# Kernel optimization log

Hardware: AMD Instinct MI355X
Metric: run time of the kernel (lower is better)

Reference implementation:

```python
import jax, jax.numpy as jnp
import numpy as np

B, T, C = 4, 1024, 1024
NH, L, DHR, FF = 16, 512, 64, 4096
DK = C // NH  # 64
EPS = 1e-6
NEG = -9e15


def rms_norm(x, w):
    var = jnp.mean(jnp.square(x), axis=-1, keepdims=True)
    return x * jax.lax.rsqrt(var + EPS) * w


def rope_apply(x):
    # Faithful to RoPE module: freq = t+1, pos pairs repeated, theta = exp(-2*pos/C*ln(1e4))
    b, t, c = x.shape
    xf = x.astype(jnp.float32)
    freq = jnp.arange(t, dtype=jnp.float32)[:, None] + 1.0           # [t,1]
    pos = jnp.arange(c // 2, dtype=jnp.float32)[:, None]
    pos = jnp.repeat(pos, 2, axis=-1).reshape(1, -1)                 # [1,c] -> p0,p0,p1,p1,...
    theta = jnp.exp(-2.0 * pos / c * jnp.log(10000.0))
    cos = jnp.cos(freq * theta)                                      # [t,c]
    sin = jnp.sin(freq * theta)
    x2 = xf.reshape(b, t, c // 2, 2)
    rot = jnp.stack([-x2[..., 1], x2[..., 0]], axis=-1).reshape(b, t, c)
    return (xf * cos + rot * sin).astype(x.dtype)


def setup_inputs() -> dict:
    key = jax.random.key(0)
    ks = jax.random.split(key, 12)
    s = 0.02
    return {
        "x": jax.random.normal(ks[0], (B, T, C), jnp.float32),
        "rms1": jnp.ones((C,), jnp.float32),
        "rms2": jnp.ones((C,), jnp.float32),
        "W_dkv": s * jax.random.normal(ks[1], (C, 2 * L), jnp.float32),
        "b_dkv": jnp.zeros((2 * L,), jnp.float32),
        "W_kr": s * jax.random.normal(ks[2], (2 * L, DHR), jnp.float32),
        "b_kr": jnp.zeros((DHR,), jnp.float32),
        "W_qr": s * jax.random.normal(ks[3], (2 * L, DHR * NH), jnp.float32),
        "b_qr": jnp.zeros((DHR * NH,), jnp.float32),
        "W_kv": s * jax.random.normal(ks[4], (L, 2 * C), jnp.float32),
        "b_kv": jnp.zeros((2 * C,), jnp.float32),
        "W_q": s * jax.random.normal(ks[5], (L, C), jnp.float32),
        "b_q": jnp.zeros((C,), jnp.float32),
        "W_o": s * jax.random.normal(ks[6], (C, C), jnp.float32),
        "b_o": jnp.zeros((C,), jnp.float32),
        "W_f1": s * jax.random.normal(ks[7], (C, FF), jnp.float32),
        "b_f1": jnp.zeros((FF,), jnp.float32),
        "W_f2": s * jax.random.normal(ks[8], (FF, C), jnp.float32),
        "b_f2": jnp.zeros((C,), jnp.float32),
    }


def mla(x, W_dkv, b_dkv, W_kr, b_kr, W_qr, b_qr, W_kv, b_kv, W_q, b_q, W_o, b_o):
    b, t, c = x.shape
    comp = jnp.einsum('btc,cd->btd', x, W_dkv) + b_dkv               # [B,T,2L]
    cKV, cq = jnp.split(comp, 2, axis=-1)                            # [B,T,L] each
    # RoPE branches (computed from the compressed representation, as in source)
    kR = rope_apply(jnp.einsum('btl,ld->btd', comp, W_kr) + b_kr)    # [B,T,DHR]
    qR = rope_apply(jnp.einsum('btl,ld->btd', comp, W_qr) + b_qr)    # roped over full NH*DHR dim
    qR = qR.reshape(b, t, NH, DHR).transpose(0, 2, 1, 3)             # [B,NH,T,DHR]
    kv = jnp.einsum('btl,ld->btd', cKV, W_kv) + b_kv
    k, v = jnp.split(kv, 2, axis=-1)                                 # [B,T,C] each
    q = jnp.einsum('btl,ld->btd', cq, W_q) + b_q                     # [B,T,C]
    to_heads = lambda z: z.reshape(b, t, NH, DK).transpose(0, 2, 1, 3)
    q, k, v = to_heads(q), to_heads(k), to_heads(v)                  # [B,NH,T,DK]
    q = jnp.concatenate([q, qR], axis=-1)                            # [B,NH,T,DK+DHR]
    k = jnp.concatenate([k, jnp.broadcast_to(kR[:, None], (b, NH, t, DHR))], axis=-1)
    # manual masked softmax in fp32, scale uses DK (not DK+DHR), faithful to source
    scale = 1.0 / np.sqrt(DK)
    w = jnp.einsum('bnqd,bnkd->bnqk', q.astype(jnp.float32), k.astype(jnp.float32)) * scale
    mask = jnp.tril(jnp.ones((t, t), jnp.float32))
    w = jnp.where(mask == 0, NEG, w)
    p = jax.nn.softmax(w, axis=-1)
    o = jnp.einsum('bnqk,bnkd->bnqd', p, v.astype(jnp.float32)).astype(x.dtype)
    o = o.transpose(0, 2, 1, 3).reshape(b, t, c)
    return jnp.einsum('btc,cd->btd', o, W_o) + b_o


def ffn(x, W_f1, b_f1, W_f2, b_f2):
    h = jax.nn.gelu(jnp.einsum('btc,cf->btf', x, W_f1) + b_f1)
    return jnp.einsum('btf,fc->btc', h, W_f2) + b_f2


def reference(x, rms1, rms2, W_dkv, b_dkv, W_kr, b_kr, W_qr, b_qr,
              W_kv, b_kv, W_q, b_q, W_o, b_o, W_f1, b_f1, W_f2, b_f2):
    h = x + mla(rms_norm(x, rms1), W_dkv, b_dkv, W_kr, b_kr, W_qr, b_qr,
                W_kv, b_kv, W_q, b_q, W_o, b_o)
    out = h + ffn(rms_norm(h, rms2), W_f1, b_f1, W_f2, b_f2)
    return out
```

## Files before the change

kernel.cpp:

```cpp
#include <hip/hip_runtime.h>

typedef unsigned int u32;
typedef unsigned short u16;
typedef __bf16 bf16x8 __attribute__((ext_vector_type(8)));
typedef float f32x4 __attribute__((ext_vector_type(4)));

#define B_ 4
#define T_ 1024
#define C_ 1024
#define NH_ 16
#define L_ 512
#define DHR_ 64
#define FF_ 4096

typedef __attribute__((address_space(3))) u32 as3_u32;
typedef __attribute__((address_space(1))) u32 as1_u32;

__device__ __forceinline__ void gld16(const u16* g, u16* l) {
  __builtin_amdgcn_global_load_lds((const as1_u32*)g, (as3_u32*)l, 16, 0, 0);
}

__device__ __forceinline__ float bf2f(u16 u) {
  union { u32 i; float f; } v; v.i = ((u32)u) << 16; return v.f;
}
__device__ __forceinline__ u16 f2bf(float f) {
  union { float f; u32 i; } v; v.f = f;
  u32 r = (v.i + 0x7FFFu + ((v.i >> 16) & 1u)) >> 16;
  return (u16)r;
}

struct TransArgs {
  const float* src[8];
  u16* dst[8];
  int R[8], C[8];
  int base[9];
};

__global__ void transpose_all(TransArgs ta) {
  __shared__ float tile[32][33];
  const int bid = blockIdx.x;
  int w = 0;
#pragma unroll
  for (int i = 1; i < 8; i++) w += (bid >= ta.base[i]);
  const int local = bid - ta.base[w];
  const int R = ta.R[w], C = ta.C[w];
  const int ctiles = C >> 5;
  const int bx = (local % ctiles) * 32;
  const int by = (local / ctiles) * 32;
  const float* in = ta.src[w];
  u16* outp = ta.dst[w];
  const int tx = threadIdx.x, ty = threadIdx.y;
  for (int i = ty; i < 32; i += 8)
    tile[i][tx] = in[(size_t)(by + i) * C + bx + tx];
  __syncthreads();
  for (int i = ty; i < 32; i += 8)
    outp[(size_t)(bx + i) * R + by + tx] = f2bf(tile[tx][i]);
}

__global__ __launch_bounds__(256) void rmsnorm_kernel(const float* __restrict__ xin,
                                                      const float* __restrict__ w,
                                                      u16* __restrict__ outp) {
  const int row = blockIdx.x;
  const int tid = threadIdx.x;
  const float* xp = xin + (size_t)row * C_;
  float v[4];
#pragma unroll
  for (int i = 0; i < 4; i++) v[i] = xp[tid + 256 * i];
  float ss = v[0] * v[0] + v[1] * v[1] + v[2] * v[2] + v[3] * v[3];
#pragma unroll
  for (int o = 32; o > 0; o >>= 1) ss += __shfl_down(ss, o, 64);
  __shared__ float red[4];
  if ((tid & 63) == 0) red[tid >> 6] = ss;
  __syncthreads();
  ss = red[0] + red[1] + red[2] + red[3];
  float scale = rsqrtf(ss * (1.0f / 1024.0f) + 1e-6f);
  u16* op = outp + (size_t)row * C_;
#pragma unroll
  for (int i = 0; i < 4; i++)
    op[tid + 256 * i] = f2bf(v[i] * scale * w[tid + 256 * i]);
}

template<int EPI, bool NCLIP>
__device__ __forceinline__ void g128_body(
    u16* As, u16* Bs,
    const u16* __restrict__ A, int lda, int aoff,
    const u16* __restrict__ BT, const float* __restrict__ bias,
    const float* __restrict__ resid, void* __restrict__ out,
    int N, int Kfull, int Klen, int m0, int n0, int koff) {
  const int tid = threadIdx.x;
  const int wave = tid >> 6, lane = tid & 63;
  const int wm = wave >> 1, wn = wave & 1;
  const int quad = lane >> 4, l15 = lane & 15;
  const int row = tid >> 2, seg = tid & 3;

  const u16* aP = A + (size_t)(m0 + row) * lda + aoff + koff + seg * 8;
  const u16* bP = BT + (size_t)(n0 + row) * Kfull + koff + seg * 8;
  u16* aL = As + row * 32 + seg * 8;
  u16* bL = Bs + row * 32 + seg * 8;
  const size_t aStep = (size_t)64 * lda;
  const size_t bStep = (size_t)64 * Kfull;

  f32x4 acc[4][4] = {};

  for (int k0 = 0; k0 < Klen; k0 += 32) {
    gld16(aP + k0, aL);
    gld16(aP + k0 + aStep, aL + 64 * 32);
    gld16(bP + k0, bL);
    gld16(bP + k0 + bStep, bL + 64 * 32);
    __syncthreads();
    bf16x8 af[4], bf[4];
#pragma unroll
    for (int mt = 0; mt < 4; mt++)
      af[mt] = *(const bf16x8*)&As[(wm * 64 + mt * 16 + l15) * 32 + quad * 8];
#pragma unroll
    for (int nt = 0; nt < 4; nt++)
      bf[nt] = *(const bf16x8*)&Bs[(wn * 64 + nt * 16 + l15) * 32 + quad * 8];
#pragma unroll
    for (int mt = 0; mt < 4; mt++)
#pragma unroll
      for (int nt = 0; nt < 4; nt++)
        acc[mt][nt] = __builtin_amdgcn_mfma_f32_16x16x32_bf16(af[mt], bf[nt], acc[mt][nt], 0, 0, 0);
    __syncthreads();
  }

#pragma unroll
  for (int nt = 0; nt < 4; nt++) {
    const int gn = n0 + wn * 64 + nt * 16 + l15;
    if (NCLIP && gn >= N) continue;
    const float bvv = (EPI == 4) ? 0.0f : bias[gn];
#pragma unroll
    for (int mt = 0; mt < 4; mt++) {
#pragma unroll
      for (int i = 0; i < 4; i++) {
        const int gm = m0 + wm * 64 + mt * 16 + quad * 4 + i;
        const size_t oidx = (size_t)gm * N + gn;
        float v = acc[mt][nt][i] + bvv;
        if (EPI == 2) {
          float xg = v;
          v = 0.5f * xg * (1.0f + tanhf(0.7978845608028654f * (xg + 0.044715f * xg * xg * xg)));
        }
        if (EPI == 3) v += resid[oidx];
        if (EPI == 1 || EPI == 3 || EPI == 4) ((float*)out)[oidx] = v;
        else ((u16*)out)[oidx] = f2bf(v);
      }
    }
  }
}

template<int EPI>
__global__ __launch_bounds__(256) void gemm128(
    const u16* __restrict__ A, int lda, int aoff,
    const u16* __restrict__ BT, const float* __restrict__ bias,
    const float* __restrict__ resid, void* __restrict__ out,
    int M, int N, int K) {
  __shared__ __align__(16) u16 As[128 * 32];
  __shared__ __align__(16) u16 Bs[128 * 32];
  g128_body<EPI, false>(As, Bs, A, lda, aoff, BT, bias, resid, out,
                        N, K, K, blockIdx.x * 128, blockIdx.y * 128, 0);
}

__global__ __launch_bounds__(256) void gemm128_splitk(
    const u16* __restrict__ A, int lda, const u16* __restrict__ BT,
    float* __restrict__ part, int N, int Kfull, int Klen) {
  __shared__ __align__(16) u16 As[128 * 32];
  __shared__ __align__(16) u16 Bs[128 * 32];
  const int z = blockIdx.z;
  g128_body<4, false>(As, Bs, A, lda, 0, BT, nullptr, nullptr,
                      part + (size_t)z * 4096 * N,
                      N, Kfull, Klen, blockIdx.x * 128, blockIdx.y * 128, z * Klen);
}

__global__ __launch_bounds__(256) void f2_reduce(
    const float* __restrict__ part, const float* __restrict__ h,
    const float* __restrict__ bias, float* __restrict__ out) {
  const size_t base = (size_t)blockIdx.x * 1024;
  const size_t PS = (size_t)4096 * 1024;
#pragma unroll
  for (int i = 0; i < 4; i++) {
    const int col = threadIdx.x + 256 * i;
    out[base + col] = h[base + col] + bias[col] + part[base + col] +
                      part[PS + base + col] + part[2 * PS + base + col] +
                      part[3 * PS + base + col];
  }
}

__global__ __launch_bounds__(256) void proj_fused(
    const u16* __restrict__ comp,
    const u16* __restrict__ WT_qr, const float* __restrict__ b_qr, float* __restrict__ qr_pre,
    const u16* __restrict__ WT_kr, const float* __restrict__ b_kr, float* __restrict__ kr_pre,
    const u16* __restrict__ WT_kv, const float* __restrict__ b_kv, u16* __restrict__ kvbuf,
    const u16* __restrict__ WT_q, const float* __restrict__ b_q, u16* __restrict__ qbuf) {
  __shared__ __align__(16) u16 As[128 * 32];
  __shared__ __align__(16) u16 Bs[128 * 32];
  const int m0 = blockIdx.x * 128;
  const int ny = blockIdx.y;
  if (ny < 8)
    g128_body<1, false>(As, Bs, comp, 1024, 0, WT_qr, b_qr, nullptr, qr_pre, 1024, 1024, 1024, m0, ny * 128, 0);
  else if (ny == 8)
    g128_body<1, true>(As, Bs, comp, 1024, 0, WT_kr, b_kr, nullptr, kr_pre, 64, 1024, 1024, m0, 0, 0);
  else if (ny < 25)
    g128_body<0, false>(As, Bs, comp, 1024, 0, WT_kv, b_kv, nullptr, kvbuf, 2048, 512, 512, m0, (ny - 9) * 128, 0);
  else
    g128_body<0, false>(As, Bs, comp, 1024, 512, WT_q, b_q, nullptr, qbuf, 1024, 512, 512, m0, (ny - 25) * 128, 0);
}

__global__ __launch_bounds__(256) void rope_build(
    const u16* __restrict__ qb, const float* __restrict__ qr_pre,
    const u16* __restrict__ kvb, const float* __restrict__ kr_pre,
    u16* __restrict__ Qf, u16* __restrict__ Kf) {
  const int bt = blockIdx.x;
  const int b = bt >> 10, t = bt & 1023;
  const float freq = (float)(t + 1);
  for (int idx = threadIdx.x; idx < 2048; idx += 256) {
    const int h = idx >> 7, d = idx & 127;
    const size_t dst = (((size_t)(b * 16 + h)) * T_ + t) * 128 + d;
    u16 qv, kvv;
    if (d < 64) {
      qv = qb[(size_t)bt * C_ + h * 64 + d];
      kvv = kvb[(size_t)bt * 2048 + h * 64 + d];
    } else {
      const int dd = d - 64;
      {
        const int g = h * 64 + dd;
        const int p = g >> 1;
        const float theta = __expf(-(float)(2 * p) * (9.210340372f / 1024.0f));
        float s, c;
        sincosf(freq * theta, &s, &c);
        const float x0 = qr_pre[(size_t)bt * 1024 + (p << 1)];
        const float x1 = qr_pre[(size_t)bt * 1024 + (p << 1) + 1];
        qv = f2bf((g & 1) ? (x1 * c + x0 * s) : (x0 * c - x1 * s));
      }
      {
        const int p = dd >> 1;
        const float theta = __expf(-(float)(2 * p) * (9.210340372f / 64.0f));
        float s, c;
        sincosf(freq * theta, &s, &c);
        const float x0 = kr_pre[(size_t)bt * 64 + (p << 1)];
        const float x1 = kr_pre[(size_t)bt * 64 + (p << 1) + 1];
        kvv = f2bf((dd & 1) ? (x1 * c + x0 * s) : (x0 * c - x1 * s));
      }
    }
    Qf[dst] = qv;
    Kf[dst] = kvv;
  }
}

__global__ __launch_bounds__(256) void vtrans_kernel(
    const u16* __restrict__ kvb, u16* __restrict__ Vf) {
  __shared__ u16 tile[64][72];
  const int bh = blockIdx.x, t0 = blockIdx.y * 64;
  const int b = bh >> 4, h = bh & 15;
  const int r = threadIdx.x >> 2, seg = (threadIdx.x & 3) * 16;
  const u16* src = &kvb[((size_t)(b * 1024) + t0 + r) * 2048 + 1024 + h * 64 + seg];
  *(uint4*)&tile[r][seg] = *(const uint4*)src;
  *(uint4*)&tile[r][seg + 8] = *(const uint4*)(src + 8);
  __syncthreads();
  const int d = threadIdx.x >> 2, ts = (threadIdx.x & 3) * 16;
  u16 tmp[16];
#pragma unroll
  for (int j = 0; j < 16; j++) tmp[j] = tile[ts + j][d];
  u16* dst = &Vf[((size_t)bh * 64 + d) * 1024 + t0 + ts];
  *(uint4*)dst = *(uint4*)tmp;
  *(uint4*)(dst + 8) = *(uint4*)(tmp + 8);
}

#define KSTR 136
#define VSTR 72

__device__ __forceinline__ void attn_tile(
    u16* Ks, u16* Vt, u16* Ps,
    const u16* __restrict__ Qf, const u16* __restrict__ Kf,
    const u16* __restrict__ Vf, u16* __restrict__ attn_o,
    int b, int h, int qt) {
  const int tid = threadIdx.x;
  const int wave = tid >> 6, lane = tid & 63;
  const int quad = lane >> 4, l15 = lane & 15;
  const int q0 = qt * 64;
  const size_t bh = (size_t)(b * 16 + h);

  bf16x8 qfrag[4];
  {
    const u16* qb = &Qf[(bh * T_ + q0 + wave * 16 + l15) * 128 + quad * 8];
#pragma unroll
    for (int kc = 0; kc < 4; kc++) qfrag[kc] = *(const bf16x8*)(qb + kc * 32);
  }

  f32x4 acc_o[4] = {};
  float m_i[4], l_i[4];
#pragma unroll
  for (int i = 0; i < 4; i++) { m_i[i] = -3.0e38f; l_i[i] = 0.0f; }

  const int kr_ = tid >> 3, kcs = (tid & 7) * 16;
  const int vd = tid >> 2, vts = (tid & 3) * 16;
  u16* Pw = Ps + wave * 16 * VSTR;

  for (int kt = 0; kt <= qt; kt++) {
    __syncthreads();
    {
      const u16* s0 = &Kf[(bh * T_ + kt * 64 + kr_) * 128 + kcs];
      const u16* s1 = s0 + 32 * 128;
      *(uint4*)&Ks[kr_ * KSTR + kcs] = *(const uint4*)s0;
      *(uint4*)&Ks[kr_ * KSTR + kcs + 8] = *(const uint4*)(s0 + 8);
      *(uint4*)&Ks[(kr_ + 32) * KSTR + kcs] = *(const uint4*)s1;
      *(uint4*)&Ks[(kr_ + 32) * KSTR + kcs + 8] = *(const uint4*)(s1 + 8);
      const u16* vs = &Vf[(bh * 64 + vd) * 1024 + kt * 64 + vts];
      *(uint4*)&Vt[vd * VSTR + vts] = *(const uint4*)vs;
      *(uint4*)&Vt[vd * VSTR + vts + 8] = *(const uint4*)(vs + 8);
    }
    __syncthreads();

    f32x4 acc_s[4] = {};
#pragma unroll
    for (int kc = 0; kc < 4; kc++) {
#pragma unroll
      for (int ng = 0; ng < 4; ng++) {
        bf16x8 bb = *(const bf16x8*)&Ks[(ng * 16 + l15) * KSTR + kc * 32 + quad * 8];
        acc_s[ng] = __builtin_amdgcn_mfma_f32_16x16x32_bf16(qfrag[kc], bb, acc_s[ng], 0, 0, 0);
      }
    }

    float sv[4][4];
#pragma unroll
    for (int ng = 0; ng < 4; ng++)
#pragma unroll
      for (int i = 0; i < 4; i++) {
        float s = acc_s[ng][i] * 0.125f;
        if (kt == qt && (ng * 16 + l15) > (wave * 16 + quad * 4 + i)) s = -3.0e38f;
        sv[ng][i] = s;
      }

    float alpha[4], mx[4];
#pragma unroll
    for (int i = 0; i < 4; i++) {
      float m = fmaxf(fmaxf(sv[0][i], sv[1][i]), fmaxf(sv[2][i], sv[3][i]));
#pragma unroll
      for (int off = 1; off < 16; off <<= 1) m = fmaxf(m, __shfl_xor(m, off, 64));
      float mn = fmaxf(m_i[i], m);
      alpha[i] = __expf(m_i[i] - mn);
      m_i[i] = mn;
      mx[i] = mn;
    }
    float rs[4] = {0.f, 0.f, 0.f, 0.f};
#pragma unroll
    for (int ng = 0; ng < 4; ng++)
#pragma unroll
      for (int i = 0; i < 4; i++) {
        float p = __expf(sv[ng][i] - mx[i]);
        rs[i] += p;
        Pw[(quad * 4 + i) * VSTR + ng * 16 + l15] = f2bf(p);
      }
#pragma unroll
    for (int i = 0; i < 4; i++) {
      float r = rs[i];
#pragma unroll
      for (int off = 1; off < 16; off <<= 1) r += __shfl_xor(r, off, 64);
      l_i[i] = l_i[i] * alpha[i] + r;
    }

#pragma unroll
    for (int ng = 0; ng < 4; ng++)
#pragma unroll
      for (int i = 0; i < 4; i++) acc_o[ng][i] *= alpha[i];
#pragma unroll
    for (int kc = 0; kc < 2; kc++) {
      bf16x8 a = *(const bf16x8*)&Pw[l15 * VSTR + kc * 32 + quad * 8];
#pragma unroll
      for (int ng = 0; ng < 4; ng++) {
        bf16x8 bb = *(const bf16x8*)&Vt[(ng * 16 + l15) * VSTR + kc * 32 + quad * 8];
        acc_o[ng] = __builtin_amdgcn_mfma_f32_16x16x32_bf16(a, bb, acc_o[ng], 0, 0, 0);
      }
    }
  }

  float linv[4];
#pragma unroll
  for (int i = 0; i < 4; i++) linv[i] = 1.0f / l_i[i];
#pragma unroll
  for (int ng = 0; ng < 4; ng++)
#pragma unroll
    for (int i = 0; i < 4; i++) {
      const int qrow = q0 + wave * 16 + quad * 4 + i;
      attn_o[((size_t)(b * T_) + qrow) * C_ + h * 64 + ng * 16 + l15] =
          f2bf(acc_o[ng][i] * linv[i]);
    }
}

__global__ __launch_bounds__(256) void attn_mfma(
    const u16* __restrict__ Qf, const u16* __restrict__ Kf,
    const u16* __restrict__ Vf, u16* __restrict__ attn_o) {
  __shared__ __align__(16) u16 Ks[64 * KSTR];
  __shared__ __align__(16) u16 Vt[64 * VSTR];
  __shared__ __align__(16) u16 Ps[4 * 16 * VSTR];
  const int j = blockIdx.x & 7;
  const int h = (blockIdx.x >> 3) & 15;
  const int b = blockIdx.x >> 7;
  attn_tile(Ks, Vt, Ps, Qf, Kf, Vf, attn_o, b, h, 15 - j);
  attn_tile(Ks, Vt, Ps, Qf, Kf, Vf, attn_o, b, h, j);
}

extern "C" void kernel_launch(void* const* d_in, const int* in_sizes, int n_in,
                              void* d_out, int out_size, void* d_ws, size_t ws_size,
                              hipStream_t stream) {
  const float* x = (const float*)d_in[0];
  const float* rms1 = (const float*)d_in[1];
  const float* rms2 = (const float*)d_in[2];
  const float* W_dkv = (const float*)d_in[3];
  const float* b_dkv = (const float*)d_in[4];
  const float* W_kr = (const float*)d_in[5];
  const float* b_kr = (const float*)d_in[6];
  const float* W_qr = (const float*)d_in[7];
  const float* b_qr = (const float*)d_in[8];
  const float* W_kv = (const float*)d_in[9];
  const float* b_kv = (const float*)d_in[10];
  const float* W_q = (const float*)d_in[11];
  const float* b_q = (const float*)d_in[12];
  const float* W_o = (const float*)d_in[13];
  const float* b_o = (const float*)d_in[14];
  const float* W_f1 = (const float*)d_in[15];
  const float* b_f1 = (const float*)d_in[16];
  const float* W_f2 = (const float*)d_in[17];
  const float* b_f2 = (const float*)d_in[18];
  float* out = (float*)d_out;

  char* ws = (char*)d_ws;
  size_t off = 0;
  auto alloc = [&](size_t bytes) -> void* {
    void* p = ws + off;
    off += (bytes + 255) & ~(size_t)255;
    return p;
  };
  u16* WT_dkv = (u16*)alloc((size_t)1024 * 1024 * 2);
  u16* WT_kr  = (u16*)alloc((size_t)128 * 1024 * 2);
  u16* WT_qr  = (u16*)alloc((size_t)1024 * 1024 * 2);
  u16* WT_kv  = (u16*)alloc((size_t)2048 * 512 * 2);
  u16* WT_q   = (u16*)alloc((size_t)1024 * 512 * 2);
  u16* WT_o   = (u16*)alloc((size_t)1024 * 1024 * 2);
  u16* WT_f1  = (u16*)alloc((size_t)4096 * 1024 * 2);
  u16* WT_f2  = (u16*)alloc((size_t)1024 * 4096 * 2);
  u16* xn1    = (u16*)alloc((size_t)4096 * 1024 * 2);
  u16* comp   = (u16*)alloc((size_t)4096 * 1024 * 2);
  float* kr_pre = (float*)alloc((size_t)4096 * 64 * 4);
  float* qr_pre = (float*)alloc((size_t)4096 * 1024 * 4);
  u16* kvbuf  = (u16*)alloc((size_t)4096 * 2048 * 2);
  u16* qbuf   = (u16*)alloc((size_t)4096 * 1024 * 2);
  u16* Qf     = (u16*)alloc((size_t)64 * 1024 * 128 * 2);
  u16* Kf     = (u16*)alloc((size_t)64 * 1024 * 128 * 2);
  u16* Vf     = (u16*)alloc((size_t)64 * 64 * 1024 * 2);
  u16* attn_o = (u16*)alloc((size_t)4096 * 1024 * 2);
  alloc((size_t)4096 * 1024 * 4);
  float* hbuf = (float*)alloc((size_t)4096 * 1024 * 4);
  u16* hn     = (u16*)alloc((size_t)4096 * 1024 * 2);
  u16* hid    = (u16*)alloc((size_t)4096 * 4096 * 2);
  float* partial = (float*)Qf;

  TransArgs ta;
  const float* srcs[8] = {W_dkv, W_kr, W_qr, W_kv, W_q, W_o, W_f1, W_f2};
  u16* dsts[8] = {WT_dkv, WT_kr, WT_qr, WT_kv, WT_q, WT_o, WT_f1, WT_f2};
  const int Rs[8] = {1024, 1024, 1024, 512, 512, 1024, 1024, 4096};
  const int Cs[8] = {1024, 64, 1024, 2048, 1024, 1024, 4096, 1024};
  int acc_t = 0;
  for (int i = 0; i < 8; i++) {
    ta.src[i] = srcs[i]; ta.dst[i] = dsts[i]; ta.R[i] = Rs[i]; ta.C[i] = Cs[i];
    ta.base[i] = acc_t;
    acc_t += (Rs[i] >> 5) * (Cs[i] >> 5);
  }
  ta.base[8] = acc_t;
  transpose_all<<<acc_t, dim3(32, 8), 0, stream>>>(ta);

  rmsnorm_kernel<<<4096, 256, 0, stream>>>(x, rms1, xn1);

  gemm128<0><<<dim3(32, 8), 256, 0, stream>>>(xn1, 1024, 0, WT_dkv, b_dkv, nullptr, comp, 4096, 1024, 1024);

  proj_fused<<<dim3(32, 33), 256, 0, stream>>>(comp,
      WT_qr, b_qr, qr_pre, WT_kr, b_kr, kr_pre,
      WT_kv, b_kv, kvbuf, WT_q, b_q, qbuf);

  rope_build<<<4096, 256, 0, stream>>>(qbuf, qr_pre, kvbuf, kr_pre, Qf, Kf);
  vtrans_kernel<<<dim3(64, 16), 256, 0, stream>>>(kvbuf, Vf);

  attn_mfma<<<B_ * NH_ * 8, 256, 0, stream>>>(Qf, Kf, Vf, attn_o);

  gemm128<3><<<dim3(32, 8), 256, 0, stream>>>(attn_o, 1024, 0, WT_o, b_o, x, hbuf, 4096, 1024, 1024);

  rmsnorm_kernel<<<4096, 256, 0, stream>>>(hbuf, rms2, hn);

  gemm128<2><<<dim3(32, 32), 256, 0, stream>>>(hn, 1024, 0, WT_f1, b_f1, nullptr, hid, 4096, 4096, 1024);

  gemm128_splitk<<<dim3(32, 8, 4), 256, 0, stream>>>(hid, 4096, WT_f2, partial, 1024, 4096, 1024);
  f2_reduce<<<4096, 256, 0, stream>>>(partial, hbuf, b_f2, out);
}
```

Measured before the change: 471.5 us.

## Fuse small kernels, narrow N-tile for 1024-wide GEMMs, cheaper GELU epilogue

Merges the first rmsnorm into the weight-transpose launch and folds the V transpose into the rope kernel, removing two launches. Adds an NT template so the 1024-wide GEMMs (dkv, out-proj) use 128x64 tiles, doubling block count to 512 for better CU fill. Rewrites GELU's tanh form as an exp-based expression and reorders the epilogue loops so bias loads are hoisted. The exp form clamps its argument and may differ slightly in rounding from tanhf.

```diff
diff --git a/kernel.cpp b/kernel.cpp
--- a/kernel.cpp
+++ b/kernel.cpp
@@ -34,11 +34,35 @@
   u16* dst[8];
   int R[8], C[8];
   int base[9];
+  const float* x;
+  const float* rmsw;
+  u16* xn;
 };
 
-__global__ void transpose_all(TransArgs ta) {
+__global__ void pre_all(TransArgs ta) {
+  const int bid = blockIdx.x;
+  if (bid >= ta.base[8]) {
+    const int row = bid - ta.base[8];
+    const int tid = threadIdx.y * 32 + threadIdx.x;
+    const float* xp = ta.x + (size_t)row * C_;
+    float v[4];
+#pragma unroll
+    for (int i = 0; i < 4; i++) v[i] = xp[tid + 256 * i];
+    float ss = v[0] * v[0] + v[1] * v[1] + v[2] * v[2] + v[3] * v[3];
+#pragma unroll
+    for (int o = 32; o > 0; o >>= 1) ss += __shfl_down(ss, o, 64);
+    __shared__ float red[4];
+    if ((tid & 63) == 0) red[tid >> 6] = ss;
+    __syncthreads();
+    ss = red[0] + red[1] + red[2] + red[3];
+    float scale = rsqrtf(ss * (1.0f / 1024.0f) + 1e-6f);
+    u16* op = ta.xn + (size_t)row * C_;
+#pragma unroll
+    for (int i = 0; i < 4; i++)
+      op[tid + 256 * i] = f2bf(v[i] * scale * ta.rmsw[tid + 256 * i]);
+    return;
+  }
   __shared__ float tile[32][33];
-  const int bid = blockIdx.x;
   int w = 0;
 #pragma unroll
   for (int i = 1; i < 8; i++) w += (bid >= ta.base[i]);
@@ -80,8 +104,8 @@
     op[tid + 256 * i] = f2bf(v[i] * scale * w[tid + 256 * i]);
 }
 
-template<int EPI, bool NCLIP>
-__device__ __forceinline__ void g128_body(
+template<int EPI, bool NCLIP, int NT>
+__device__ __forceinline__ void g_body(
     u16* As, u16* Bs,
     const u16* __restrict__ A, int lda, int aoff,
     const u16* __restrict__ BT, const float* __restrict__ bias,
@@ -100,44 +124,51 @@
   const size_t aStep = (size_t)64 * lda;
   const size_t bStep = (size_t)64 * Kfull;
 
-  f32x4 acc[4][4] = {};
+  f32x4 acc[4][NT] = {};
 
   for (int k0 = 0; k0 < Klen; k0 += 32) {
     gld16(aP + k0, aL);
     gld16(aP + k0 + aStep, aL + 64 * 32);
     gld16(bP + k0, bL);
-    gld16(bP + k0 + bStep, bL + 64 * 32);
+    if (NT == 4) gld16(bP + k0 + bStep, bL + 64 * 32);
     __syncthreads();
-    bf16x8 af[4], bf[4];
+    bf16x8 af[4], bfr[NT];
 #pragma unroll
     for (int mt = 0; mt < 4; mt++)
       af[mt] = *(const bf16x8*)&As[(wm * 64 + mt * 16 + l15) * 32 + quad * 8];
 #pragma unroll
-    for (int nt = 0; nt < 4; nt++)
-      bf[nt] = *(const bf16x8*)&Bs[(wn * 64 + nt * 16 + l15) * 32 + quad * 8];
+    for (int nt = 0; nt < NT; nt++)
+      bfr[nt] = *(const bf16x8*)&Bs[(wn * (NT * 16) + nt * 16 + l15) * 32 + quad * 8];
 #pragma unroll
     for (int mt = 0; mt < 4; mt++)
 #pragma unroll
-      for (int nt = 0; nt < 4; nt++)
-        acc[mt][nt] = __builtin_amdgcn_mfma_f32_16x16x32_bf16(af[mt], bf[nt], acc[mt][nt], 0, 0, 0);
+      for (int nt = 0; nt < NT; nt++)
+        acc[mt][nt] = __builtin_amdgcn_mfma_f32_16x16x32_bf16(af[mt], bfr[nt], acc[mt][nt], 0, 0, 0);
     __syncthreads();
   }
 
-#pragma unroll
-  for (int nt = 0; nt < 4; nt++) {
-    const int gn = n0 + wn * 64 + nt * 16 + l15;
-    if (NCLIP && gn >= N) continue;
-    const float bvv = (EPI == 4) ? 0.0f : bias[gn];
-#pragma unroll
-    for (int mt = 0; mt < 4; mt++) {
-#pragma unroll
-      for (int i = 0; i < 4; i++) {
-        const int gm = m0 + wm * 64 + mt * 16 + quad * 4 + i;
-        const size_t oidx = (size_t)gm * N + gn;
-        float v = acc[mt][nt][i] + bvv;
+  float bvv[NT];
+#pragma unroll
+  for (int nt = 0; nt < NT; nt++) {
+    const int gn = n0 + wn * (NT * 16) + nt * 16 + l15;
+    bvv[nt] = (EPI == 4) ? 0.0f : ((NCLIP && gn >= N) ? 0.0f : bias[gn]);
+  }
+#pragma unroll
+  for (int mt = 0; mt < 4; mt++) {
+#pragma unroll
+    for (int i = 0; i < 4; i++) {
+      const int gm = m0 + wm * 64 + mt * 16 + quad * 4 + i;
+      const size_t rowb = (size_t)gm * N;
+#pragma unroll
+      for (int nt = 0; nt < NT; nt++) {
+        const int gn = n0 + wn * (NT * 16) + nt * 16 + l15;
+        if (NCLIP && gn >= N) continue;
+        const size_t oidx = rowb + gn;
+        float v = acc[mt][nt][i] + bvv[nt];
         if (EPI == 2) {
-          float xg = v;
-          v = 0.5f * xg * (1.0f + tanhf(0.7978845608028654f * (xg + 0.044715f * xg * xg * xg)));
+          float y = 0.7978845608028654f * (v + 0.044715f * v * v * v);
+          float t = __expf(fminf(2.0f * y, 80.0f));
+          v = v * t / (t + 1.0f);
         }
         if (EPI == 3) v += resid[oidx];
         if (EPI == 1 || EPI == 3 || EPI == 4) ((float*)out)[oidx] = v;
@@ -147,16 +178,16 @@
   }
 }
 
-template<int EPI>
-__global__ __launch_bounds__(256) void gemm128(
+template<int EPI, int NT>
+__global__ __launch_bounds__(256) void gemmN(
     const u16* __restrict__ A, int lda, int aoff,
     const u16* __restrict__ BT, const float* __restrict__ bias,
     const float* __restrict__ resid, void* __restrict__ out,
-    int M, int N, int K) {
+    int N, int K) {
   __shared__ __align__(16) u16 As[128 * 32];
-  __shared__ __align__(16) u16 Bs[128 * 32];
-  g128_body<EPI, false>(As, Bs, A, lda, aoff, BT, bias, resid, out,
-                        N, K, K, blockIdx.x * 128, blockIdx.y * 128, 0);
+  __shared__ __align__(16) u16 Bs[NT * 32 * 32];
+  g_body<EPI, false, NT>(As, Bs, A, lda, aoff, BT, bias, resid, out,
+                         N, K, K, blockIdx.x * 128, blockIdx.y * (NT * 32), 0);
 }
 
 __global__ __launch_bounds__(256) void gemm128_splitk(
@@ -165,7 +196,7 @@
   __shared__ __align__(16) u16 As[128 * 32];
   __shared__ __align__(16) u16 Bs[128 * 32];
   const int z = blockIdx.z;
-  g128_body<4, false>(As, Bs, A, lda, 0, BT, nullptr, nullptr,
+  g_body<4, false, 4>(As, Bs, A, lda, 0, BT, nullptr, nullptr,
                       part + (size_t)z * 4096 * N,
                       N, Kfull, Klen, blockIdx.x * 128, blockIdx.y * 128, z * Klen);
 }
@@ -195,19 +226,38 @@
   const int m0 = blockIdx.x * 128;
   const int ny = blockIdx.y;
   if (ny < 8)
-    g128_body<1, false>(As, Bs, comp, 1024, 0, WT_qr, b_qr, nullptr, qr_pre, 1024, 1024, 1024, m0, ny * 128, 0);
+    g_body<1, false, 4>(As, Bs, comp, 1024, 0, WT_qr, b_qr, nullptr, qr_pre, 1024, 1024, 1024, m0, ny * 128, 0);
   else if (ny == 8)
-    g128_body<1, true>(As, Bs, comp, 1024, 0, WT_kr, b_kr, nullptr, kr_pre, 64, 1024, 1024, m0, 0, 0);
+    g_body<1, true, 4>(As, Bs, comp, 1024, 0, WT_kr, b_kr, nullptr, kr_pre, 64, 1024, 1024, m0, 0, 0);
   else if (ny < 25)
-    g128_body<0, false>(As, Bs, comp, 1024, 0, WT_kv, b_kv, nullptr, kvbuf, 2048, 512, 512, m0, (ny - 9) * 128, 0);
+    g_body<0, false, 4>(As, Bs, comp, 1024, 0, WT_kv, b_kv, nullptr, kvbuf, 2048, 512, 512, m0, (ny - 9) * 128, 0);
   else
-    g128_body<0, false>(As, Bs, comp, 1024, 512, WT_q, b_q, nullptr, qbuf, 1024, 512, 512, m0, (ny - 25) * 128, 0);
-}
-
-__global__ __launch_bounds__(256) void rope_build(
+    g_body<0, false, 4>(As, Bs, comp, 1024, 512, WT_q, b_q, nullptr, qbuf, 1024, 512, 512, m0, (ny - 25) * 128, 0);
+}
+
+__global__ __launch_bounds__(256) void rope_vtrans(
     const u16* __restrict__ qb, const float* __restrict__ qr_pre,
     const u16* __restrict__ kvb, const float* __restrict__ kr_pre,
-    u16* __restrict__ Qf, u16* __restrict__ Kf) {
+    u16* __restrict__ Qf, u16* __restrict__ Kf, u16* __restrict__ Vf) {
+  __shared__ u16 tile[64][72];
+  if (blockIdx.x >= 4096) {
+    const int bid2 = blockIdx.x - 4096;
+    const int bh = bid2 & 63, t0 = (bid2 >> 6) * 64;
+    const int b = bh >> 4, h = bh & 15;
+    const int r = threadIdx.x >> 2, seg = (threadIdx.x & 3) * 16;
+    const u16* src = &kvb[((size_t)(b * 1024) + t0 + r) * 2048 + 1024 + h * 64 + seg];
+    *(uint4*)&tile[r][seg] = *(const uint4*)src;
+    *(uint4*)&tile[r][seg + 8] = *(const uint4*)(src + 8);
+    __syncthreads();
+    const int d = threadIdx.x >> 2, ts = (threadIdx.x & 3) * 16;
+    u16 tmp[16];
+#pragma unroll
+    for (int j = 0; j < 16; j++) tmp[j] = tile[ts + j][d];
+    u16* dst = &Vf[((size_t)bh * 64 + d) * 1024 + t0 + ts];
+    *(uint4*)dst = *(uint4*)tmp;
+    *(uint4*)(dst + 8) = *(uint4*)(tmp + 8);
+    return;
+  }
   const int bt = blockIdx.x;
   const int b = bt >> 10, t = bt & 1023;
   const float freq = (float)(t + 1);
@@ -243,25 +293,6 @@
     Qf[dst] = qv;
     Kf[dst] = kvv;
   }
-}
-
-__global__ __launch_bounds__(256) void vtrans_kernel(
-    const u16* __restrict__ kvb, u16* __restrict__ Vf) {
-  __shared__ u16 tile[64][72];
-  const int bh = blockIdx.x, t0 = blockIdx.y * 64;
-  const int b = bh >> 4, h = bh & 15;
-  const int r = threadIdx.x >> 2, seg = (threadIdx.x & 3) * 16;
-  const u16* src = &kvb[((size_t)(b * 1024) + t0 + r) * 2048 + 1024 + h * 64 + seg];
-  *(uint4*)&tile[r][seg] = *(const uint4*)src;
-  *(uint4*)&tile[r][seg + 8] = *(const uint4*)(src + 8);
-  __syncthreads();
-  const int d = threadIdx.x >> 2, ts = (threadIdx.x & 3) * 16;
-  u16 tmp[16];
-#pragma unroll
-  for (int j = 0; j < 16; j++) tmp[j] = tile[ts + j][d];
-  u16* dst = &Vf[((size_t)bh * 64 + d) * 1024 + t0 + ts];
-  *(uint4*)dst = *(uint4*)tmp;
-  *(uint4*)(dst + 8) = *(uint4*)(tmp + 8);
 }
 
 #define KSTR 136
@@ -465,26 +496,24 @@
     acc_t += (Rs[i] >> 5) * (Cs[i] >> 5);
   }
   ta.base[8] = acc_t;
-  transpose_all<<<acc_t, dim3(32, 8), 0, stream>>>(ta);
-
-  rmsnorm_kernel<<<4096, 256, 0, stream>>>(x, rms1, xn1);
-
-  gemm128<0><<<dim3(32, 8), 256, 0, stream>>>(xn1, 1024, 0, WT_dkv, b_dkv, nullptr, comp, 4096, 1024, 1024);
+  ta.x = x; ta.rmsw = rms1; ta.xn = xn1;
+  pre_all<<<acc_t + 4096, dim3(32, 8), 0, stream>>>(ta);
+
+  gemmN<0, 2><<<dim3(32, 16), 256, 0, stream>>>(xn1, 1024, 0, WT_dkv, b_dkv, nullptr, comp, 1024, 1024);
 
   proj_fused<<<dim3(32, 33), 256, 0, stream>>>(comp,
       WT_qr, b_qr, qr_pre, WT_kr, b_kr, kr_pre,
       WT_kv, b_kv, kvbuf, WT_q, b_q, qbuf);
 
-  rope_build<<<4096, 256, 0, stream>>>(qbuf, qr_pre, kvbuf, kr_pre, Qf, Kf);
-  vtrans_kernel<<<dim3(64, 16), 256, 0, stream>>>(kvbuf, Vf);
+  rope_vtrans<<<4096 + 1024, 256, 0, stream>>>(qbuf, qr_pre, kvbuf, kr_pre, Qf, Kf, Vf);
 
   attn_mfma<<<B_ * NH_ * 8, 256, 0, stream>>>(Qf, Kf, Vf, attn_o);
 
-  gemm128<3><<<dim3(32, 8), 256, 0, stream>>>(attn_o, 1024, 0, WT_o, b_o, x, hbuf, 4096, 1024, 1024);
+  gemmN<3, 2><<<dim3(32, 16), 256, 0, stream>>>(attn_o, 1024, 0, WT_o, b_o, x, hbuf, 1024, 1024);
 
   rmsnorm_kernel<<<4096, 256, 0, stream>>>(hbuf, rms2, hn);
 
-  gemm128<2><<<dim3(32, 32), 256, 0, stream>>>(hn, 1024, 0, WT_f1, b_f1, nullptr, hid, 4096, 4096, 1024);
+  gemmN<2, 4><<<dim3(32, 32), 256, 0, stream>>>(hn, 1024, 0, WT_f1, b_f1, nullptr, hid, 4096, 1024);
 
   gemm128_splitk<<<dim3(32, 8, 4), 256, 0, stream>>>(hid, 4096, WT_f2, partial, 1024, 4096, 1024);
   f2_reduce<<<4096, 256, 0, stream>>>(partial, hbuf, b_f2, out);
```

Measured after the change: 445.0 us. 5.6% less time.
